# Performance work log

Measured on AMD Instinct MI355X. Metric: run time of the kernel, lower is better.

Reference implementation:

```python
import jax, jax.numpy as jnp
import numpy as np

# Hyperparameters (from init_kwargs)
D_MODEL = 1024
D_STATE = 64
HEADDIM = 64
MIMO_RANK = 2
CHUNK = 128
EXPAND = 2
D_INNER = EXPAND * D_MODEL            # 2048
NHEADS = D_INNER // HEADDIM           # 32
G = MIMO_RANK * D_STATE               # effective state channels per head = 128
D_CONV = 4
D_XBC = D_INNER + 2 * NHEADS * G      # conv channels
D_IN_PROJ = 2 * D_INNER + 2 * NHEADS * G + NHEADS  # [z, x, B, C, dt]


def rmsnorm(x, w, eps=1e-5):
    return x * w * jax.lax.rsqrt(jnp.mean(x * x, axis=-1, keepdims=True) + eps)


def setup_inputs() -> dict:
    key = jax.random.key(0)
    ks = jax.random.split(key, 8)
    B, L = 2, 2048
    x = jax.random.normal(ks[0], (B, L, D_MODEL), jnp.float32)
    norm_w = jnp.ones((D_MODEL,), jnp.float32)
    in_proj_w = jax.random.normal(ks[1], (D_IN_PROJ, D_MODEL), jnp.float32) * 0.02
    conv_w = jax.random.normal(ks[2], (D_XBC, D_CONV), jnp.float32) * 0.2
    conv_b = jnp.zeros((D_XBC,), jnp.float32)
    dt_bias = jax.random.uniform(ks[3], (NHEADS,), jnp.float32, minval=-4.0, maxval=-1.0)
    A_log = jnp.log(jax.random.uniform(ks[4], (NHEADS,), jnp.float32, minval=1.0, maxval=8.0))
    D_skip = jnp.ones((NHEADS,), jnp.float32)
    gnorm_w = jnp.ones((D_INNER,), jnp.float32)
    out_proj_w = jax.random.normal(ks[5], (D_MODEL, D_INNER), jnp.float32) * 0.02
    return dict(x=x, norm_w=norm_w, in_proj_w=in_proj_w, conv_w=conv_w, conv_b=conv_b,
                dt_bias=dt_bias, A_log=A_log, D_skip=D_skip, gnorm_w=gnorm_w,
                out_proj_w=out_proj_w)


def _mamba3(u, in_proj_w, conv_w, conv_b, dt_bias, A_log, D_skip, gnorm_w, out_proj_w):
    B, L, _ = u.shape
    H, P = NHEADS, HEADDIM
    nc = L // CHUNK

    zxbcdt = u @ in_proj_w.T                                   # (B,L,D_IN_PROJ)
    z, xbc, dt_raw = jnp.split(zxbcdt, [D_INNER, D_INNER + D_XBC], axis=-1)

    # causal depthwise conv (width D_CONV) + SiLU on [x, B, C]
    xp = jnp.pad(xbc, ((0, 0), (D_CONV - 1, 0), (0, 0)))
    conv = conv_b + sum(xp[:, k:k + L, :] * conv_w[:, k] for k in range(D_CONV))
    xbc = jax.nn.silu(conv)
    xh, Bm, Cm = jnp.split(xbc, [D_INNER, D_INNER + H * G], axis=-1)

    Xc = xh.reshape(B, nc, CHUNK, H, P)
    Bc = Bm.reshape(B, nc, CHUNK, H, G)
    Cc = Cm.reshape(B, nc, CHUNK, H, G)

    dt = jax.nn.softplus(dt_raw + dt_bias)                     # (B,L,H), positive
    A = -jnp.exp(A_log)                                        # (H,), negative
    dtc = dt.reshape(B, nc, CHUNK, H)
    a = dtc * A                                                # log decay, (B,nc,cs,H)
    cum = jnp.cumsum(a, axis=2)                                # inclusive cumsum within chunk

    # intra-chunk (quadratic, causal) part
    cumT = cum.transpose(0, 1, 3, 2)                           # (B,nc,H,cs)
    diff = cumT[..., :, None] - cumT[..., None, :]             # cum_l - cum_s
    mask = jnp.tril(jnp.ones((CHUNK, CHUNK), bool))
    decay = jnp.where(mask, jnp.exp(jnp.where(mask, diff, 0.0)), 0.0)
    dtT = dtc.transpose(0, 1, 3, 2)                            # (B,nc,H,cs)
    scores = jnp.einsum('bclhg,bcshg->bchls', Cc, Bc) * decay * dtT[:, :, :, None, :]
    Y_intra = jnp.einsum('bchls,bcshp->bclhp', scores, Xc)

    # inter-chunk state recurrence
    w = jnp.exp(cum[:, :, -1:, :] - cum) * dtc                 # (B,nc,cs,H)
    S = jnp.einsum('bcshg,bcshp->bchgp', Bc * w[..., None], Xc)  # chunk states
    dlast = jnp.exp(cum[:, :, -1, :])                          # (B,nc,H) total chunk decay

    def step(carry, inp):
        dl, s = inp
        return dl[:, :, None, None] * carry + s, carry

    init = jnp.zeros((B, H, G, P), u.dtype)
    _, Hprev = jax.lax.scan(step, init, (dlast.transpose(1, 0, 2), S.transpose(1, 0, 2, 3, 4)))
    Hprev = Hprev.transpose(1, 0, 2, 3, 4)                     # (B,nc,H,G,P) state before chunk
    Y_inter = jnp.einsum('bclhg,bchgp->bclhp', Cc * jnp.exp(cum)[..., None], Hprev)

    y = (Y_intra + Y_inter + D_skip[:, None] * Xc).reshape(B, L, D_INNER)
    y = rmsnorm(y * jax.nn.silu(z), gnorm_w)                   # gated RMSNorm
    return y @ out_proj_w.T


def reference(x, norm_w, in_proj_w, conv_w, conv_b, dt_bias, A_log, D_skip, gnorm_w, out_proj_w):
    # pre-norm residual wrapper
    return x + _mamba3(rmsnorm(x, norm_w), in_proj_w, conv_w, conv_b,
                       dt_bias, A_log, D_skip, gnorm_w, out_proj_w)
```

## Files before the change

kernel.cpp:

```cpp
#include <hip/hip_runtime.h>

typedef unsigned short u16;
typedef __attribute__((ext_vector_type(8))) short bf16x8;
typedef __attribute__((ext_vector_type(4))) float f32x4;

#define MFMA16(a,b,c) __builtin_amdgcn_mfma_f32_16x16x32_bf16(a,b,c,0,0,0)

#define DMODEL   1024
#define DINNER   2048
#define NHEADS   32
#define HEADDIM  64
#define GDIM     128
#define DXBC     10240
#define DPROJ    12320
#define CHUNK_L  128
#define NCHUNK   16
#define NROWS    4096

__device__ __forceinline__ float b2f(u16 u){ return __uint_as_float(((unsigned)u)<<16); }
__device__ __forceinline__ u16 f2b(float f){
  unsigned u = __float_as_uint(f);
  u += 0x7fffu + ((u>>16)&1u);
  return (u16)(u>>16);
}

__device__ __forceinline__ void gload_lds16(const void* g, void* l){
  __builtin_amdgcn_global_load_lds(
      (const __attribute__((address_space(1))) unsigned int*)g,
      (__attribute__((address_space(3))) unsigned int*)l, 16, 0, 0);
}

__global__ void k_f32_to_bf16_2(const float* __restrict__ s1, u16* __restrict__ d1, int n1,
                                const float* __restrict__ s2, u16* __restrict__ d2, int n2){
  int i = blockIdx.x*blockDim.x + threadIdx.x;
  int stride = gridDim.x*blockDim.x;
  int t1 = n1 >> 2, t2 = n2 >> 2;
  for (int j=i; j<t1+t2; j+=stride){
    const float4* sp; uint2* dp; int idx;
    if (j < t1){ sp = (const float4*)s1; dp = (uint2*)d1; idx = j; }
    else       { sp = (const float4*)s2; dp = (uint2*)d2; idx = j - t1; }
    float4 v = sp[idx];
    uint2 o;
    o.x = (unsigned)f2b(v.x) | ((unsigned)f2b(v.y)<<16);
    o.y = (unsigned)f2b(v.z) | ((unsigned)f2b(v.w)<<16);
    dp[idx] = o;
  }
}

__global__ __launch_bounds__(256) void k_rmsnorm_in(const float* __restrict__ x,
                                                    const float* __restrict__ w,
                                                    u16* __restrict__ u){
  int row = blockIdx.x, tid = threadIdx.x;
  float4 v = reinterpret_cast<const float4*>(x + (size_t)row*DMODEL)[tid];
  float ss = v.x*v.x + v.y*v.y + v.z*v.z + v.w*v.w;
  #pragma unroll
  for (int off=32; off>0; off>>=1) ss += __shfl_down(ss, off, 64);
  __shared__ float red[4];
  if ((tid&63)==0) red[tid>>6] = ss;
  __syncthreads();
  float tot = red[0]+red[1]+red[2]+red[3];
  float sc = rsqrtf(tot/(float)DMODEL + 1e-5f);
  float4 wv = reinterpret_cast<const float4*>(w)[tid];
  uint2 o;
  o.x = (unsigned)f2b(v.x*wv.x*sc) | ((unsigned)f2b(v.y*wv.y*sc)<<16);
  o.y = (unsigned)f2b(v.z*wv.z*sc) | ((unsigned)f2b(v.w*wv.w*sc)<<16);
  reinterpret_cast<uint2*>(u + (size_t)row*DMODEL)[tid] = o;
}

__global__ __launch_bounds__(512) void k_gemm1_8p(const u16* __restrict__ A,
                                                  const u16* __restrict__ W,
                                                  u16* __restrict__ zb,
                                                  u16* __restrict__ xbc){
  __shared__ __align__(16) u16 lds[65536];
  const int tid  = threadIdx.x;
  const int lane = tid & 63, w = tid >> 6;
  const int wr = w >> 2, wc = w & 3;
  int bid = blockIdx.x;
  int xcd = bid & 7, g = bid >> 3;
  int st  = xcd*6 + (g >> 4);
  int wi  = g & 15;
  int tm  = (st/12)*4 + (wi>>2);
  int tn  = (st%12)*4 + (wi&3);
  const int m0 = tm*256, n0 = tn*256;

  const int srow = w*8 + (lane>>3);
  const int scol = ((lane&7) ^ ((lane>>3)&7))*8;
  const u16* aS = A + (size_t)(m0 + srow)*DMODEL + scol;
  const u16* bS = W + (size_t)(n0 + srow)*DMODEL + scol;
  const int ldsw = w*512;

  const int rr = lane & 15, gq = lane >> 4;

  f32x4 acc[8][4];
  #pragma unroll
  for (int i=0;i<8;i++)
    #pragma unroll
    for (int j=0;j<4;j++) acc[i][j] = (f32x4){0,0,0,0};

  auto SU_A = [&](int kt, int j){
    gload_lds16(aS + (size_t)(j*64)*DMODEL + kt*64,
                lds + (kt&1)*32768 + j*4096 + ldsw);
  };
  auto SU_B = [&](int kt, int j){
    gload_lds16(bS + (size_t)(j*64)*DMODEL + kt*64,
                lds + (kt&1)*32768 + 16384 + j*4096 + ldsw);
  };

  SU_A(0,0); SU_A(0,2); SU_B(0,0); SU_B(0,2); SU_B(0,1); SU_B(0,3); SU_A(0,1); SU_A(0,3);
  asm volatile("s_waitcnt vmcnt(2)" ::: "memory");
  __builtin_amdgcn_s_barrier();
  __builtin_amdgcn_sched_barrier(0);

  for (int kt = 0; kt < 16; ++kt){
    const u16* bufA = lds + (kt&1)*32768;
    const u16* bufB = bufA + 16384;
    const bool stg = (kt < 15);
    bf16x8 af[4][2], bw0[2][2], bw1[2][2];

    auto RDA = [&](int ti, int ks)->bf16x8{
      int r = wr*128 + ti*16 + rr;
      int s = (ks*4 + gq) ^ (rr & 7);
      return *(const bf16x8*)&bufA[r*64 + s*8];
    };
    auto RDB = [&](int tj, int ks)->bf16x8{
      int r = wc*64 + tj*16 + rr;
      int s = (ks*4 + gq) ^ (rr & 7);
      return *(const bf16x8*)&bufB[r*64 + s*8];
    };

    #pragma unroll
    for (int ti=0;ti<4;ti++){ af[ti][0]=RDA(ti,0); af[ti][1]=RDA(ti,1); }
    #pragma unroll
    for (int tj=0;tj<2;tj++){ bw0[tj][0]=RDB(tj,0); bw0[tj][1]=RDB(tj,1); }
    if (stg){ SU_A(kt+1,0); SU_A(kt+1,2); }
    __builtin_amdgcn_s_barrier();
    asm volatile("s_waitcnt lgkmcnt(0)" ::: "memory");
    __builtin_amdgcn_sched_barrier(0);
    __builtin_amdgcn_s_setprio(1);
    #pragma unroll
    for (int ti=0;ti<4;ti++)
      #pragma unroll
      for (int tj=0;tj<2;tj++){
        acc[ti][tj] = MFMA16(af[ti][0], bw0[tj][0], acc[ti][tj]);
        acc[ti][tj] = MFMA16(af[ti][1], bw0[tj][1], acc[ti][tj]);
      }
    __builtin_amdgcn_s_setprio(0);
    __builtin_amdgcn_s_barrier();

    #pragma unroll
    for (int tj=0;tj<2;tj++){ bw1[tj][0]=RDB(tj+2,0); bw1[tj][1]=RDB(tj+2,1); }
    if (stg){ SU_B(kt+1,0); SU_B(kt+1,2); }
    __builtin_amdgcn_s_barrier();
    asm volatile("s_waitcnt lgkmcnt(0)" ::: "memory");
    __builtin_amdgcn_sched_barrier(0);
    __builtin_amdgcn_s_setprio(1);
    #pragma unroll
    for (int ti=0;ti<4;ti++)
      #pragma unroll
      for (int tj=0;tj<2;tj++){
        acc[ti][tj+2] = MFMA16(af[ti][0], bw1[tj][0], acc[ti][tj+2]);
        acc[ti][tj+2] = MFMA16(af[ti][1], bw1[tj][1], acc[ti][tj+2]);
      }
    __builtin_amdgcn_s_setprio(0);
    if (stg) asm volatile("s_waitcnt vmcnt(4)" ::: "memory");
    else     asm volatile("s_waitcnt vmcnt(0)" ::: "memory");
    __builtin_amdgcn_s_barrier();

    #pragma unroll
    for (int ti=0;ti<4;ti++){ af[ti][0]=RDA(ti+4,0); af[ti][1]=RDA(ti+4,1); }
    if (stg){ SU_B(kt+1,1); SU_B(kt+1,3); }
    __builtin_amdgcn_s_barrier();
    asm volatile("s_waitcnt lgkmcnt(0)" ::: "memory");
    __builtin_amdgcn_sched_barrier(0);
    __builtin_amdgcn_s_setprio(1);
    #pragma unroll
    for (int ti=0;ti<4;ti++)
      #pragma unroll
      for (int tj=0;tj<2;tj++){
        acc[4+ti][tj] = MFMA16(af[ti][0], bw0[tj][0], acc[4+ti][tj]);
        acc[4+ti][tj] = MFMA16(af[ti][1], bw0[tj][1], acc[4+ti][tj]);
      }
    __builtin_amdgcn_s_setprio(0);
    __builtin_amdgcn_s_barrier();

    if (stg){ SU_A(kt+1,1); SU_A(kt+1,3); }
    __builtin_amdgcn_s_barrier();
    __builtin_amdgcn_sched_barrier(0);
    __builtin_amdgcn_s_setprio(1);
    #pragma unroll
    for (int ti=0;ti<4;ti++)
      #pragma unroll
      for (int tj=0;tj<2;tj++){
        acc[4+ti][tj+2] = MFMA16(af[ti][0], bw1[tj][0], acc[4+ti][tj+2]);
        acc[4+ti][tj+2] = MFMA16(af[ti][1], bw1[tj][1], acc[4+ti][tj+2]);
      }
    __builtin_amdgcn_s_setprio(0);
    if (stg){
      asm volatile("s_waitcnt vmcnt(2)" ::: "memory");
      __builtin_amdgcn_s_barrier();
      __builtin_amdgcn_sched_barrier(0);
    }
  }

  const int row0 = m0 + wr*128 + (lane>>4)*4;
  const int colb = wc*64 + (lane&15);
  if (tn >= 8){
    const int cb = n0 - DINNER;
    #pragma unroll
    for (int ti=0;ti<8;ti++)
      #pragma unroll
      for (int tj=0;tj<4;tj++)
        #pragma unroll
        for (int q=0;q<4;q++)
          xbc[(size_t)(row0 + ti*16 + q)*DXBC + cb + colb + tj*16] = f2b(acc[ti][tj][q]);
  } else {
    #pragma unroll
    for (int ti=0;ti<8;ti++)
      #pragma unroll
      for (int tj=0;tj<4;tj++)
        #pragma unroll
        for (int q=0;q<4;q++)
          zb[(size_t)(row0 + ti*16 + q)*DINNER + n0 + colb + tj*16] = f2b(acc[ti][tj][q]);
  }
}

__global__ __launch_bounds__(256) void k_dtfused(const u16* __restrict__ A,
                                                 const u16* __restrict__ W,
                                                 const float* __restrict__ dt_bias,
                                                 const float* __restrict__ A_log,
                                                 float* __restrict__ dtT,
                                                 float* __restrict__ cumT){
  __shared__ float part[4][128][33];
  const int bc = blockIdx.x;
  const int tid = threadIdx.x;
  const int lane = tid & 63, wv = tid >> 6;
  const int r = lane & 15, kb = (lane>>4)*8;
  const int k0 = wv*256;
  const u16* b0p = W + (size_t)(12288 + r)*DMODEL + k0 + kb;
  const u16* b1p = b0p + (size_t)16*DMODEL;
  f32x4 acc[8][2];
  #pragma unroll
  for (int t=0;t<8;t++){ acc[t][0]=(f32x4){0,0,0,0}; acc[t][1]=(f32x4){0,0,0,0}; }
  #pragma unroll
  for (int ks=0; ks<256; ks+=32){
    bf16x8 b0 = *(const bf16x8*)(b0p + ks);
    bf16x8 b1 = *(const bf16x8*)(b1p + ks);
    #pragma unroll
    for (int ti=0;ti<8;ti++){
      bf16x8 a = *(const bf16x8*)(A + (size_t)(bc*128 + ti*16 + r)*DMODEL + k0 + kb + ks);
      acc[ti][0] = MFMA16(a,b0,acc[ti][0]);
      acc[ti][1] = MFMA16(a,b1,acc[ti][1]);
    }
  }
  #pragma unroll
  for (int ti=0;ti<8;ti++)
    #pragma unroll
    for (int cj=0;cj<2;cj++)
      #pragma unroll
      for (int q=0;q<4;q++)
        part[wv][ti*16 + (lane>>4)*4 + q][cj*16 + (lane&15)] = acc[ti][cj][q];
  __syncthreads();
  for (int i = tid; i < 128*32; i += 256){
    int s = i >> 5, h = i & 31;
    float v = part[0][s][h]+part[1][s][h]+part[2][s][h]+part[3][s][h] + dt_bias[h];
    float dt = (v > 20.f) ? v : log1pf(expf(v));
    part[0][s][h] = dt;
    part[1][s][h] = dt * (-expf(A_log[h]));
  }
  __syncthreads();
  #pragma unroll
  for (int off=1; off<128; off<<=1){
    float t[16];
    #pragma unroll
    for (int j=0;j<16;j++){
      int i = tid + j*256; int s = i>>5, h = i&31;
      t[j] = (s>=off) ? part[1][s-off][h] : 0.f;
    }
    __syncthreads();
    #pragma unroll
    for (int j=0;j<16;j++){
      int i = tid + j*256; int s = i>>5, h = i&31;
      part[1][s][h] += t[j];
    }
    __syncthreads();
  }
  for (int i = tid; i < 4096; i += 256){
    int h = i >> 7, s = i & 127;
    dtT [((size_t)bc*32 + h)*128 + s] = part[0][s][h];
    cumT[((size_t)bc*32 + h)*128 + s] = part[1][s][h];
  }
}

__global__ __launch_bounds__(256) void k_conv(const u16* __restrict__ xbc,
                                              const float* __restrict__ cw,
                                              const float* __restrict__ cb,
                                              u16* __restrict__ xh,
                                              u16* __restrict__ Bm,
                                              u16* __restrict__ Cm){
  int c  = (blockIdx.x*256 + threadIdx.x)*2;
  int row0 = blockIdx.y*16;
  int l0 = row0 & 2047;
  float4 wa = reinterpret_cast<const float4*>(cw)[c];
  float4 wb = reinterpret_cast<const float4*>(cw)[c+1];
  float cba = cb[c], cbb = cb[c+1];
  float a3=0,a2=0,a1=0, b3=0,b2=0,b1=0;
  auto loadpair = [&](int rw, float& fa, float& fb){
    unsigned v = *(const unsigned*)&xbc[(size_t)rw*DXBC + c];
    fa = b2f((u16)v); fb = b2f((u16)(v>>16));
  };
  if (l0 >= 3){
    loadpair(row0-3, a3,b3); loadpair(row0-2, a2,b2); loadpair(row0-1, a1,b1);
  }
  #pragma unroll
  for (int i=0;i<16;i++){
    float a0,b0; loadpair(row0+i, a0,b0);
    float sa = cba + a3*wa.x + a2*wa.y + a1*wa.z + a0*wa.w;
    float sb = cbb + b3*wb.x + b2*wb.y + b1*wb.z + b0*wb.w;
    sa = sa/(1.f+expf(-sa)); sb = sb/(1.f+expf(-sb));
    unsigned o = (unsigned)f2b(sa) | ((unsigned)f2b(sb)<<16);
    int rw = row0 + i;
    if (c < DINNER)            *(unsigned*)&xh[(size_t)rw*DINNER + c] = o;
    else if (c < DINNER+4096)  *(unsigned*)&Bm[(size_t)rw*4096 + (c-DINNER)] = o;
    else                       *(unsigned*)&Cm[(size_t)rw*4096 + (c-DINNER-4096)] = o;
    a3=a2; a2=a1; a1=a0; b3=b2; b2=b1; b1=b0;
  }
}

__global__ __launch_bounds__(512) void k_states(const u16* __restrict__ Bm,
                                                const u16* __restrict__ xh,
                                                const float* __restrict__ dtT,
                                                const float* __restrict__ cumT,
                                                u16* __restrict__ S){
  int blk = blockIdx.x;
  int h = blk & 31, bc = blk >> 5;
  __shared__ __align__(16) u16 Bw[128][136];
  __shared__ __align__(16) u16 XT[64][136];
  __shared__ float cum[128], dtv[128];
  int tid = threadIdx.x;
  if (tid < 128){ cum[tid] = cumT[(size_t)blk*128+tid]; dtv[tid] = dtT[(size_t)blk*128+tid]; }
  __syncthreads();
  float clast = cum[127];
  #pragma unroll
  for (int it=0; it<4; ++it){
    int s  = it*32 + (tid>>4);
    int g8 = (tid&15)*8;
    uint4 v = *(const uint4*)&Bm[(size_t)(bc*128+s)*4096 + h*128 + g8];
    float w = expf(clast - cum[s]) * dtv[s];
    const u16* pv = (const u16*)&v;
    #pragma unroll
    for (int j=0;j<8;j++) Bw[g8+j][s] = f2b(b2f(pv[j]) * w);
  }
  #pragma unroll
  for (int it=0; it<4; ++it){
    int s  = it*32 + (tid>>4);
    int p4 = (tid&15)*4;
    uint2 v = *(const uint2*)&xh[(size_t)(bc*128+s)*DINNER + h*64 + p4];
    const u16* pv = (const u16*)&v;
    #pragma unroll
    for (int j=0;j<4;j++) XT[p4+j][s] = pv[j];
  }
  __syncthreads();
  int lane = tid & 63, wv = tid >> 6;
  int r = lane & 15, kb = (lane>>4)*8;
  f32x4 acc[4];
  #pragma unroll
  for (int j=0;j<4;j++) acc[j] = (f32x4){0,0,0,0};
  #pragma unroll
  for (int k=0;k<128;k+=32){
    bf16x8 a0 = *(const bf16x8*)&Bw[wv*16 + r][k+kb];
    #pragma unroll
    for (int tj=0;tj<4;tj++){
      bf16x8 bb = *(const bf16x8*)&XT[tj*16 + r][k+kb];
      acc[tj] = MFMA16(a0,bb,acc[tj]);
    }
  }
  u16* Sp = S + (size_t)blk*8192;
  int g0 = wv*16 + (lane>>4)*4, p0 = lane&15;
  #pragma unroll
  for (int tj=0;tj<4;tj++)
    #pragma unroll
    for (int rr=0;rr<4;rr++)
      Sp[(g0 + rr)*64 + tj*16 + p0] = f2b(acc[tj][rr]);
}

__global__ __launch_bounds__(256) void k_scan(const u16* __restrict__ S,
                                              const float* __restrict__ cumT,
                                              u16* __restrict__ Hp){
  int slice = blockIdx.x & 3;
  int bh = blockIdx.x >> 2;
  int b = bh >> 5, h = bh & 31;
  int e0 = slice*2048 + threadIdx.x*8;
  float c8[8];
  #pragma unroll
  for (int j=0;j<8;j++) c8[j] = 0.f;
  for (int c=0;c<NCHUNK;c++){
    int blk = (b*16+c)*32 + h;
    float dl = expf(cumT[(size_t)blk*128 + 127]);
    uint4 sv = *(const uint4*)&S[(size_t)blk*8192 + e0];
    const u16* sp = (const u16*)&sv;
    uint4 o; u16* op = (u16*)&o;
    #pragma unroll
    for (int j=0;j<8;j++) op[j] = f2b(c8[j]);
    *reinterpret_cast<uint4*>(&Hp[(size_t)blk*8192 + e0]) = o;
    #pragma unroll
    for (int j=0;j<8;j++) c8[j] = dl*c8[j] + b2f(sp[j]);
  }
}

__global__ __launch_bounds__(512) void k_intra(const u16* __restrict__ Cm,
                                               const u16* __restrict__ Bm,
                                               const u16* __restrict__ xh,
                                               const u16* __restrict__ Hp,
                                               const float* __restrict__ dtT,
                                               const float* __restrict__ cumT,
                                               const float* __restrict__ Dskip,
                                               u16* __restrict__ yh){
  int blk = blockIdx.x;
  int h = blk & 31, bc = blk >> 5;
  __shared__ __align__(16) u16 Bl[128][136];
  __shared__ __align__(16) u16 XT[64][136];
  __shared__ __align__(16) u16 HT[64][136];
  __shared__ float cum[128], dtv[128];
  int tid = threadIdx.x;
  int lane = tid & 63, wv = tid >> 6;
  int r = lane & 15, kb = (lane>>4)*8;

  bf16x8 cfr[4];
  {
    const u16* cp = Cm + (size_t)(bc*128 + wv*16 + r)*4096 + h*128 + kb;
    #pragma unroll
    for (int ks=0;ks<4;ks++) cfr[ks] = *(const bf16x8*)(cp + ks*32);
  }

  if (tid < 128){ cum[tid] = cumT[(size_t)blk*128+tid]; dtv[tid] = dtT[(size_t)blk*128+tid]; }
  #pragma unroll
  for (int it=0; it<4; ++it){
    int rw = it*32 + (tid>>4);
    int g8 = (tid&15)*8;
    *(uint4*)&Bl[rw][g8] = *(const uint4*)&Bm[(size_t)(bc*128+rw)*4096 + h*128 + g8];
  }
  #pragma unroll
  for (int it=0; it<4; ++it){
    int s  = it*32 + (tid>>4);
    int p4 = (tid&15)*4;
    uint2 v = *(const uint2*)&xh[(size_t)(bc*128+s)*DINNER + h*64 + p4];
    const u16* pv = (const u16*)&v;
    #pragma unroll
    for (int j=0;j<4;j++) XT[p4+j][s] = pv[j];
  }
  #pragma unroll
  for (int it=0; it<4; ++it){
    int g  = it*32 + (tid>>4);
    int p4 = (tid&15)*4;
    uint2 v = *(const uint2*)&Hp[(size_t)blk*8192 + g*64 + p4];
    const u16* pv = (const u16*)&v;
    #pragma unroll
    for (int j=0;j<4;j++) HT[p4+j][g] = pv[j];
  }
  __syncthreads();
  const int tjmax = wv;

  f32x4 p1[8];
  #pragma unroll
  for (int j=0;j<8;j++) p1[j] = (f32x4){0,0,0,0};
  #pragma unroll
  for (int ks=0;ks<4;ks++){
    bf16x8 a0 = cfr[ks];
    #pragma unroll
    for (int tj=0;tj<8;tj++){
      if (tj > tjmax) continue;
      bf16x8 bb = *(const bf16x8*)&Bl[tj*16 + r][ks*32+kb];
      p1[tj] = MFMA16(a0,bb,p1[tj]);
    }
  }
  __syncthreads();
  int row0 = wv*16 + (lane>>4)*4;
  #pragma unroll
  for (int tj=0;tj<8;tj++)
    #pragma unroll
    for (int rr=0;rr<4;rr++){
      int l = row0 + rr;
      int s = tj*16 + (lane&15);
      float v = p1[tj][rr];
      v = (s <= l) ? v * expf(cum[l]-cum[s]) * dtv[s] : 0.f;
      Bl[l][s] = f2b(v);
    }
  __syncthreads();

  f32x4 y[4];
  #pragma unroll
  for (int j=0;j<4;j++) y[j] = (f32x4){0,0,0,0};
  #pragma unroll
  for (int ks=0;ks<4;ks++){
    bf16x8 a0 = cfr[ks];
    #pragma unroll
    for (int tj=0;tj<4;tj++){
      bf16x8 bb = *(const bf16x8*)&HT[tj*16 + r][ks*32+kb];
      y[tj] = MFMA16(a0,bb,y[tj]);
    }
  }
  #pragma unroll
  for (int rr=0;rr<4;rr++){
    float e = expf(cum[row0 + rr]);
    #pragma unroll
    for (int tj=0;tj<4;tj++) y[tj][rr] *= e;
  }
  #pragma unroll
  for (int k=0;k<128;k+=32){
    bf16x8 a0 = *(const bf16x8*)&Bl[wv*16 + r][k+kb];
    #pragma unroll
    for (int tj=0;tj<4;tj++){
      bf16x8 bb = *(const bf16x8*)&XT[tj*16 + r][k+kb];
      y[tj] = MFMA16(a0,bb,y[tj]);
    }
  }
  float Dh = Dskip[h];
  #pragma unroll
  for (int tj=0;tj<4;tj++)
    #pragma unroll
    for (int rr=0;rr<4;rr++){
      int l = row0 + rr;
      int p = tj*16 + (lane&15);
      float xv = b2f(XT[p][l]);
      yh[(size_t)(bc*128 + l)*DINNER + h*64 + p] = f2b(y[tj][rr] + Dh*xv);
    }
}

__global__ __launch_bounds__(256) void k_gate(const u16* __restrict__ yh,
                                              const u16* __restrict__ zb,
                                              const float* __restrict__ gw,
                                              u16* __restrict__ out){
  int row = blockIdx.x, tid = threadIdx.x;
  const uint4 yv = reinterpret_cast<const uint4*>(yh + (size_t)row*DINNER)[tid];
  const uint4 zv = reinterpret_cast<const uint4*>(zb + (size_t)row*DINNER)[tid];
  const unsigned* yp = (const unsigned*)&yv;
  const unsigned* zp = (const unsigned*)&zv;
  float t[8]; float ss = 0.f;
  #pragma unroll
  for (int i=0;i<4;i++){
    float y0 = b2f((u16)yp[i]), y1 = b2f((u16)(yp[i]>>16));
    float z0 = b2f((u16)zp[i]), z1 = b2f((u16)(zp[i]>>16));
    float v0 = y0 * (z0 / (1.f + expf(-z0)));
    float v1 = y1 * (z1 / (1.f + expf(-z1)));
    t[2*i] = v0; t[2*i+1] = v1; ss += v0*v0 + v1*v1;
  }
  #pragma unroll
  for (int off=32; off>0; off>>=1) ss += __shfl_down(ss, off, 64);
  __shared__ float red[4];
  if ((tid&63)==0) red[tid>>6] = ss;
  __syncthreads();
  float tot = red[0]+red[1]+red[2]+red[3];
  float g = rsqrtf(tot/(float)DINNER + 1e-5f);
  const float4 g0 = reinterpret_cast<const float4*>(gw)[tid*2];
  const float4 g1 = reinterpret_cast<const float4*>(gw)[tid*2+1];
  uint4 o;
  unsigned* op = (unsigned*)&o;
  float gg[8] = {g0.x,g0.y,g0.z,g0.w,g1.x,g1.y,g1.z,g1.w};
  #pragma unroll
  for (int i=0;i<4;i++)
    op[i] = (unsigned)f2b(t[2*i]*gg[2*i]*g) | ((unsigned)f2b(t[2*i+1]*gg[2*i+1]*g)<<16);
  reinterpret_cast<uint4*>(out + (size_t)row*DINNER)[tid] = o;
}

__global__ __launch_bounds__(256) void k_gemm2_64(const u16* __restrict__ A,
                                                  const u16* __restrict__ W,
                                                  const float* __restrict__ xres,
                                                  float* __restrict__ out){
  __shared__ __align__(16) u16 lds[2*16384];
  const int tid  = threadIdx.x;
  const int lane = tid & 63, wv = tid >> 6;
  const int wr = wv >> 1, wc = wv & 1;
  const int NWG = 8*32, Q = NWG/8;
  int swz = (blockIdx.x & 7)*Q + (blockIdx.x >> 3);
  int tm = swz / 8, tn = swz % 8;
  int m0 = tm*128, n0 = tn*128;
  const int K = DINNER;

  const int srow = tid >> 3;
  const int sslot = ((tid&7) ^ ((tid>>3)&7))*8;
  const u16* aSrc = A + (size_t)(m0 + srow)*K + sslot;
  const u16* bSrc = W + (size_t)(n0 + srow)*K + sslot;
  const int ldsu = wv*512;

  const int rr = lane & 15, gq = lane >> 4;

  f32x4 acc[4][4];
  #pragma unroll
  for (int i=0;i<4;i++)
    #pragma unroll
    for (int j=0;j<4;j++) acc[i][j] = (f32x4){0,0,0,0};

  auto STAGE = [&](int kt){
    u16* base = lds + (kt&1)*16384;
    #pragma unroll
    for (int j=0;j<4;j++)
      gload_lds16(aSrc + (size_t)(j*32)*K + kt*64, base + j*2048 + ldsu);
    #pragma unroll
    for (int j=0;j<4;j++)
      gload_lds16(bSrc + (size_t)(j*32)*K + kt*64, base + 8192 + j*2048 + ldsu);
  };
  auto KSTEP = [&](int kt, bool stg){
    const u16* bufA = lds + (kt&1)*16384;
    const u16* bufB = bufA + 8192;
    bf16x8 af[4][2], bw[4][2];
    #pragma unroll
    for (int t=0;t<4;t++){
      #pragma unroll
      for (int ks=0;ks<2;ks++){
        int sa = (ks*4 + gq) ^ (rr & 7);
        af[t][ks] = *(const bf16x8*)&bufA[(wr*64 + t*16 + rr)*64 + sa*8];
        bw[t][ks] = *(const bf16x8*)&bufB[(wc*64 + t*16 + rr)*64 + sa*8];
      }
    }
    asm volatile("s_waitcnt lgkmcnt(0)" ::: "memory");
    __builtin_amdgcn_s_barrier();
    if (stg) STAGE(kt+2);
    __builtin_amdgcn_s_setprio(1);
    #pragma unroll
    for (int ti=0;ti<4;ti++)
      #pragma unroll
      for (int tj=0;tj<4;tj++){
        acc[ti][tj] = MFMA16(af[ti][0], bw[tj][0], acc[ti][tj]);
        acc[ti][tj] = MFMA16(af[ti][1], bw[tj][1], acc[ti][tj]);
      }
    __builtin_amdgcn_s_setprio(0);
  };

  STAGE(0); STAGE(1);
  asm volatile("s_waitcnt vmcnt(8)" ::: "memory");
  __builtin_amdgcn_s_barrier();
  __builtin_amdgcn_sched_barrier(0);
  const int NT = K/64;
  for (int kt = 0; kt < NT-2; ++kt){
    KSTEP(kt, true);
    asm volatile("s_waitcnt vmcnt(8)" ::: "memory");
    __builtin_amdgcn_s_barrier();
    __builtin_amdgcn_sched_barrier(0);
  }
  KSTEP(NT-2, false);
  asm volatile("s_waitcnt vmcnt(0)" ::: "memory");
  __builtin_amdgcn_s_barrier();
  __builtin_amdgcn_sched_barrier(0);
  KSTEP(NT-1, false);

  int row0 = m0 + wr*64 + (lane>>4)*4;
  int col0 = n0 + wc*64 + (lane&15);
  #pragma unroll
  for (int ti=0;ti<4;ti++)
    #pragma unroll
    for (int tj=0;tj<4;tj++)
      #pragma unroll
      for (int q=0;q<4;q++){
        size_t idx = (size_t)(row0+ti*16+q)*DMODEL + col0 + tj*16;
        out[idx] = acc[ti][tj][q] + xres[idx];
      }
}

extern "C" void kernel_launch(void* const* d_in, const int* in_sizes, int n_in,
                              void* d_out, int out_size, void* d_ws, size_t ws_size,
                              hipStream_t stream) {
  (void)in_sizes; (void)n_in; (void)out_size; (void)ws_size;
  const float* x         = (const float*)d_in[0];
  const float* norm_w    = (const float*)d_in[1];
  const float* in_proj_w = (const float*)d_in[2];
  const float* conv_w    = (const float*)d_in[3];
  const float* conv_b    = (const float*)d_in[4];
  const float* dt_bias   = (const float*)d_in[5];
  const float* A_log     = (const float*)d_in[6];
  const float* D_skip    = (const float*)d_in[7];
  const float* gnorm_w   = (const float*)d_in[8];
  const float* out_proj_w= (const float*)d_in[9];
  float* out = (float*)d_out;

  char* ws = (char*)d_ws;
  size_t off = 0;
  auto alloc = [&](size_t bytes)->char*{
    char* p = ws + off; off = (off + bytes + 255) & ~(size_t)255; return p;
  };
  u16*   W2    = (u16*)  alloc((size_t)DMODEL*DINNER*2);
  u16*   zb    = (u16*)  alloc((size_t)NROWS*DINNER*2);
  float* dtT   = (float*)alloc((size_t)1024*128*4);
  float* cumT  = (float*)alloc((size_t)1024*128*4);
  u16*   xhb   = (u16*)  alloc((size_t)NROWS*DINNER*2);
  u16*   Bmb   = (u16*)  alloc((size_t)NROWS*4096*2);
  u16*   Cmb   = (u16*)  alloc((size_t)NROWS*4096*2);
  char*  R1    = alloc((size_t)NROWS*DXBC*2);
  u16*   xbcr  = (u16*)R1;
  u16*   S     = (u16*)R1;
  u16*   Hp    = (u16*)(R1 + (size_t)1024*8192*4);
  u16*   yh    = (u16*)R1;
  char*  R2    = alloc((size_t)DPROJ*DMODEL*2 + (size_t)NROWS*DMODEL*2);
  u16*   W1    = (u16*)R2;
  u16*   u_bf  = (u16*)(R2 + (size_t)DPROJ*DMODEL*2);
  u16*   gated = (u16*)R2;

  k_f32_to_bf16_2<<<2048,256,0,stream>>>(in_proj_w, W1, DPROJ*DMODEL,
                                         out_proj_w, W2, DMODEL*DINNER);
  k_rmsnorm_in<<<NROWS,256,0,stream>>>(x, norm_w, u_bf);
  k_gemm1_8p<<<768,512,0,stream>>>(u_bf, W1, zb, xbcr);
  k_dtfused<<<32,256,0,stream>>>(u_bf, W1, dt_bias, A_log, dtT, cumT);
  k_conv<<<dim3(DXBC/512, NROWS/16),256,0,stream>>>(xbcr, conv_w, conv_b, xhb, Bmb, Cmb);
  k_states<<<1024,512,0,stream>>>(Bmb, xhb, dtT, cumT, S);
  k_scan<<<256,256,0,stream>>>(S, cumT, Hp);
  k_intra<<<1024,512,0,stream>>>(Cmb, Bmb, xhb, Hp, dtT, cumT, D_skip, yh);
  k_gate<<<NROWS,256,0,stream>>>(yh, zb, gnorm_w, gated);
  k_gemm2_64<<<8*32,256,0,stream>>>(gated, W2, x, out);
}
```

Measured before the change: 310.3 us.

## Fuse weight conversion with input RMSNorm and split dt projection into GEMM plus scan

```diff
diff --git a/kernel.cpp b/kernel.cpp
--- a/kernel.cpp
+++ b/kernel.cpp
@@ -30,41 +30,41 @@
       (__attribute__((address_space(3))) unsigned int*)l, 16, 0, 0);
 }
 
-__global__ void k_f32_to_bf16_2(const float* __restrict__ s1, u16* __restrict__ d1, int n1,
-                                const float* __restrict__ s2, u16* __restrict__ d2, int n2){
-  int i = blockIdx.x*blockDim.x + threadIdx.x;
-  int stride = gridDim.x*blockDim.x;
-  int t1 = n1 >> 2, t2 = n2 >> 2;
-  for (int j=i; j<t1+t2; j+=stride){
-    const float4* sp; uint2* dp; int idx;
-    if (j < t1){ sp = (const float4*)s1; dp = (uint2*)d1; idx = j; }
-    else       { sp = (const float4*)s2; dp = (uint2*)d2; idx = j - t1; }
-    float4 v = sp[idx];
+__global__ __launch_bounds__(256) void k_prep(const float* __restrict__ s1, u16* __restrict__ d1, int n1,
+                                              const float* __restrict__ s2, u16* __restrict__ d2, int n2,
+                                              const float* __restrict__ x, const float* __restrict__ w,
+                                              u16* __restrict__ u){
+  __shared__ float red[4];
+  if (blockIdx.x < 2048){
+    int i = blockIdx.x*256 + threadIdx.x;
+    int stride = 2048*256;
+    int t1 = n1 >> 2, t2 = n2 >> 2;
+    for (int j=i; j<t1+t2; j+=stride){
+      const float4* sp; uint2* dp; int idx;
+      if (j < t1){ sp = (const float4*)s1; dp = (uint2*)d1; idx = j; }
+      else       { sp = (const float4*)s2; dp = (uint2*)d2; idx = j - t1; }
+      float4 v = sp[idx];
+      uint2 o;
+      o.x = (unsigned)f2b(v.x) | ((unsigned)f2b(v.y)<<16);
+      o.y = (unsigned)f2b(v.z) | ((unsigned)f2b(v.w)<<16);
+      dp[idx] = o;
+    }
+  } else {
+    int row = blockIdx.x - 2048, tid = threadIdx.x;
+    float4 v = reinterpret_cast<const float4*>(x + (size_t)row*DMODEL)[tid];
+    float ss = v.x*v.x + v.y*v.y + v.z*v.z + v.w*v.w;
+    #pragma unroll
+    for (int off=32; off>0; off>>=1) ss += __shfl_down(ss, off, 64);
+    if ((tid&63)==0) red[tid>>6] = ss;
+    __syncthreads();
+    float tot = red[0]+red[1]+red[2]+red[3];
+    float sc = rsqrtf(tot/(float)DMODEL + 1e-5f);
+    float4 wv = reinterpret_cast<const float4*>(w)[tid];
     uint2 o;
-    o.x = (unsigned)f2b(v.x) | ((unsigned)f2b(v.y)<<16);
-    o.y = (unsigned)f2b(v.z) | ((unsigned)f2b(v.w)<<16);
-    dp[idx] = o;
-  }
-}
-
-__global__ __launch_bounds__(256) void k_rmsnorm_in(const float* __restrict__ x,
-                                                    const float* __restrict__ w,
-                                                    u16* __restrict__ u){
-  int row = blockIdx.x, tid = threadIdx.x;
-  float4 v = reinterpret_cast<const float4*>(x + (size_t)row*DMODEL)[tid];
-  float ss = v.x*v.x + v.y*v.y + v.z*v.z + v.w*v.w;
-  #pragma unroll
-  for (int off=32; off>0; off>>=1) ss += __shfl_down(ss, off, 64);
-  __shared__ float red[4];
-  if ((tid&63)==0) red[tid>>6] = ss;
-  __syncthreads();
-  float tot = red[0]+red[1]+red[2]+red[3];
-  float sc = rsqrtf(tot/(float)DMODEL + 1e-5f);
-  float4 wv = reinterpret_cast<const float4*>(w)[tid];
-  uint2 o;
-  o.x = (unsigned)f2b(v.x*wv.x*sc) | ((unsigned)f2b(v.y*wv.y*sc)<<16);
-  o.y = (unsigned)f2b(v.z*wv.z*sc) | ((unsigned)f2b(v.w*wv.w*sc)<<16);
-  reinterpret_cast<uint2*>(u + (size_t)row*DMODEL)[tid] = o;
+    o.x = (unsigned)f2b(v.x*wv.x*sc) | ((unsigned)f2b(v.y*wv.y*sc)<<16);
+    o.y = (unsigned)f2b(v.z*wv.z*sc) | ((unsigned)f2b(v.w*wv.w*sc)<<16);
+    reinterpret_cast<uint2*>(u + (size_t)row*DMODEL)[tid] = o;
+  }
 }
 
 __global__ __launch_bounds__(512) void k_gemm1_8p(const u16* __restrict__ A,
@@ -224,71 +224,73 @@
   }
 }
 
-__global__ __launch_bounds__(256) void k_dtfused(const u16* __restrict__ A,
+__global__ __launch_bounds__(256) void k_gemm_dt(const u16* __restrict__ A,
                                                  const u16* __restrict__ W,
-                                                 const float* __restrict__ dt_bias,
-                                                 const float* __restrict__ A_log,
-                                                 float* __restrict__ dtT,
-                                                 float* __restrict__ cumT){
-  __shared__ float part[4][128][33];
-  const int bc = blockIdx.x;
-  const int tid = threadIdx.x;
-  const int lane = tid & 63, wv = tid >> 6;
-  const int r = lane & 15, kb = (lane>>4)*8;
+                                                 float* __restrict__ dtraw){
+  const int lane = threadIdx.x & 63, wv = threadIdx.x >> 6;
+  const int m0 = blockIdx.x*32;
+  const int n0 = DINNER + DXBC;
+  const int r  = lane & 15;
+  const int kb = (lane>>4)*8;
   const int k0 = wv*256;
-  const u16* b0p = W + (size_t)(12288 + r)*DMODEL + k0 + kb;
-  const u16* b1p = b0p + (size_t)16*DMODEL;
-  f32x4 acc[8][2];
-  #pragma unroll
-  for (int t=0;t<8;t++){ acc[t][0]=(f32x4){0,0,0,0}; acc[t][1]=(f32x4){0,0,0,0}; }
-  #pragma unroll
-  for (int ks=0; ks<256; ks+=32){
-    bf16x8 b0 = *(const bf16x8*)(b0p + ks);
-    bf16x8 b1 = *(const bf16x8*)(b1p + ks);
-    #pragma unroll
-    for (int ti=0;ti<8;ti++){
-      bf16x8 a = *(const bf16x8*)(A + (size_t)(bc*128 + ti*16 + r)*DMODEL + k0 + kb + ks);
-      acc[ti][0] = MFMA16(a,b0,acc[ti][0]);
-      acc[ti][1] = MFMA16(a,b1,acc[ti][1]);
-    }
-  }
-  #pragma unroll
-  for (int ti=0;ti<8;ti++)
-    #pragma unroll
-    for (int cj=0;cj<2;cj++)
-      #pragma unroll
-      for (int q=0;q<4;q++)
-        part[wv][ti*16 + (lane>>4)*4 + q][cj*16 + (lane&15)] = acc[ti][cj][q];
+  const u16* a0p = A + (size_t)(m0 + r)*DMODEL + k0 + kb;
+  const u16* a1p = a0p + 16*DMODEL;
+  const u16* b0p = W + (size_t)(n0 + r)*DMODEL + k0 + kb;
+  const u16* b1p = b0p + 16*DMODEL;
+  f32x4 acc00={0,0,0,0}, acc01={0,0,0,0}, acc10={0,0,0,0}, acc11={0,0,0,0};
+  #pragma unroll
+  for (int k=0;k<256;k+=32){
+    bf16x8 a0 = *(const bf16x8*)(a0p + k);
+    bf16x8 a1 = *(const bf16x8*)(a1p + k);
+    bf16x8 b0 = *(const bf16x8*)(b0p + k);
+    bf16x8 b1 = *(const bf16x8*)(b1p + k);
+    acc00 = MFMA16(a0,b0,acc00);
+    acc01 = MFMA16(a0,b1,acc01);
+    acc10 = MFMA16(a1,b0,acc10);
+    acc11 = MFMA16(a1,b1,acc11);
+  }
+  __shared__ float part[4][1024];
+  int rowb = (lane>>4)*4, col = lane&15;
+  #pragma unroll
+  for (int rr=0; rr<4; rr++){
+    part[wv][(rowb+rr)*32 + col]         = acc00[rr];
+    part[wv][(rowb+rr)*32 + col+16]      = acc01[rr];
+    part[wv][(rowb+16+rr)*32 + col]      = acc10[rr];
+    part[wv][(rowb+16+rr)*32 + col+16]   = acc11[rr];
+  }
   __syncthreads();
-  for (int i = tid; i < 128*32; i += 256){
-    int s = i >> 5, h = i & 31;
-    float v = part[0][s][h]+part[1][s][h]+part[2][s][h]+part[3][s][h] + dt_bias[h];
-    float dt = (v > 20.f) ? v : log1pf(expf(v));
-    part[0][s][h] = dt;
-    part[1][s][h] = dt * (-expf(A_log[h]));
-  }
-  __syncthreads();
+  int idx = threadIdx.x*4;
+  #pragma unroll
+  for (int q=0;q<4;q++){
+    int i = idx+q;
+    dtraw[(size_t)m0*NHEADS + i] = part[0][i]+part[1][i]+part[2][i]+part[3][i];
+  }
+}
+
+__global__ __launch_bounds__(128) void k_dtscan(const float* __restrict__ dtraw,
+                                                const float* __restrict__ dt_bias,
+                                                const float* __restrict__ A_log,
+                                                float* __restrict__ dtT,
+                                                float* __restrict__ cumT){
+  int blk = blockIdx.x;
+  int h   = blk & 31;
+  int bc  = blk >> 5;
+  int s   = threadIdx.x;
+  int row = bc*128 + s;
+  float xv = dtraw[(size_t)row*NHEADS + h] + dt_bias[h];
+  float dt = (xv > 20.f) ? xv : log1pf(expf(xv));
+  float a  = dt * (-expf(A_log[h]));
+  __shared__ float lds[128];
+  lds[s] = a; __syncthreads();
   #pragma unroll
   for (int off=1; off<128; off<<=1){
-    float t[16];
-    #pragma unroll
-    for (int j=0;j<16;j++){
-      int i = tid + j*256; int s = i>>5, h = i&31;
-      t[j] = (s>=off) ? part[1][s-off][h] : 0.f;
-    }
+    float t = (s>=off) ? lds[s-off] : 0.f;
     __syncthreads();
-    #pragma unroll
-    for (int j=0;j<16;j++){
-      int i = tid + j*256; int s = i>>5, h = i&31;
-      part[1][s][h] += t[j];
-    }
+    lds[s] += t;
     __syncthreads();
   }
-  for (int i = tid; i < 4096; i += 256){
-    int h = i >> 7, s = i & 127;
-    dtT [((size_t)bc*32 + h)*128 + s] = part[0][s][h];
-    cumT[((size_t)bc*32 + h)*128 + s] = part[1][s][h];
-  }
+  dtT[(size_t)blk*128 + s]  = dt;
+  cumT[(size_t)blk*128 + s] = lds[s];
 }
 
 __global__ __launch_bounds__(256) void k_conv(const u16* __restrict__ xbc,
@@ -679,6 +681,7 @@
   };
   u16*   W2    = (u16*)  alloc((size_t)DMODEL*DINNER*2);
   u16*   zb    = (u16*)  alloc((size_t)NROWS*DINNER*2);
+  float* dtraw = (float*)alloc((size_t)NROWS*NHEADS*4);
   float* dtT   = (float*)alloc((size_t)1024*128*4);
   float* cumT  = (float*)alloc((size_t)1024*128*4);
   u16*   xhb   = (u16*)  alloc((size_t)NROWS*DINNER*2);
@@ -694,12 +697,13 @@
   u16*   u_bf  = (u16*)(R2 + (size_t)DPROJ*DMODEL*2);
   u16*   gated = (u16*)R2;
 
-  k_f32_to_bf16_2<<<2048,256,0,stream>>>(in_proj_w, W1, DPROJ*DMODEL,
-                                         out_proj_w, W2, DMODEL*DINNER);
-  k_rmsnorm_in<<<NROWS,256,0,stream>>>(x, norm_w, u_bf);
+  k_prep<<<2048+NROWS,256,0,stream>>>(in_proj_w, W1, DPROJ*DMODEL,
+                                      out_proj_w, W2, DMODEL*DINNER,
+                                      x, norm_w, u_bf);
   k_gemm1_8p<<<768,512,0,stream>>>(u_bf, W1, zb, xbcr);
-  k_dtfused<<<32,256,0,stream>>>(u_bf, W1, dt_bias, A_log, dtT, cumT);
+  k_gemm_dt<<<NROWS/32,256,0,stream>>>(u_bf, W1, dtraw);
   k_conv<<<dim3(DXBC/512, NROWS/16),256,0,stream>>>(xbcr, conv_w, conv_b, xhb, Bmb, Cmb);
+  k_dtscan<<<1024,128,0,stream>>>(dtraw, dt_bias, A_log, dtT, cumT);
   k_states<<<1024,512,0,stream>>>(Bmb, xhb, dtT, cumT, S);
   k_scan<<<256,256,0,stream>>>(S, cumT, Hp);
   k_intra<<<1024,512,0,stream>>>(Cmb, Bmb, xhb, Hp, dtT, cumT, D_skip, yh);
```

After: 293.1 us. -5.5%, faster.
